# Kernel tuning notes

Hardware: AMD Instinct MI355X
Metric: run time of the kernel (lower is better)

Reference implementation:

```python
import jax, jax.numpy as jnp
import numpy as np

# MambaConfig defaults for d_model=512
N_LAYERS = 2
D_MODEL = 512
ED = 2 * D_MODEL        # d_inner (expand_factor=2)
D_STATE = 16
D_CONV = 4
DT_RANK = D_MODEL // 16  # 32
INPUT_DIM = 64
EPS = 1e-5


def silu(v):
    return v * jax.nn.sigmoid(v)


def rmsnorm(v, w):
    return v * jax.lax.rsqrt(jnp.mean(v * v, axis=-1, keepdims=True) + EPS) * w


def setup_inputs() -> dict:
    key = jax.random.key(0)
    ks = jax.random.split(key, 12)
    B, L = 2, 2048
    s = 0.02
    x = jax.random.normal(ks[0], (B, L, INPUT_DIM), dtype=jnp.float32)
    emb_w = jax.random.normal(ks[1], (D_MODEL, INPUT_DIM), dtype=jnp.float32) * s
    emb_b = jnp.zeros((D_MODEL,), dtype=jnp.float32)
    in_proj_w = jax.random.normal(ks[2], (N_LAYERS, 2 * ED, D_MODEL), dtype=jnp.float32) * s
    conv_w = jax.random.normal(ks[3], (N_LAYERS, ED, D_CONV), dtype=jnp.float32) * 0.2
    conv_b = jax.random.normal(ks[4], (N_LAYERS, ED), dtype=jnp.float32) * 0.02
    x_proj_w = jax.random.normal(ks[5], (N_LAYERS, DT_RANK + 2 * D_STATE, ED), dtype=jnp.float32) * s
    dt_proj_w = jax.random.normal(ks[6], (N_LAYERS, ED, DT_RANK), dtype=jnp.float32) * s
    dt_proj_b = jax.random.normal(ks[7], (N_LAYERS, ED), dtype=jnp.float32) * 0.5 - 4.0  # softplus(~-4) ~ small dt
    A_log = jnp.log(jnp.tile(jnp.arange(1, D_STATE + 1, dtype=jnp.float32), (N_LAYERS, ED, 1)))  # S4D-real init
    D = jnp.ones((N_LAYERS, ED), dtype=jnp.float32)
    out_proj_w = jax.random.normal(ks[8], (N_LAYERS, D_MODEL, ED), dtype=jnp.float32) * s
    norm_w = jnp.ones((N_LAYERS, D_MODEL), dtype=jnp.float32)
    return dict(x=x, emb_w=emb_w, emb_b=emb_b, in_proj_w=in_proj_w, conv_w=conv_w,
                conv_b=conv_b, x_proj_w=x_proj_w, dt_proj_w=dt_proj_w, dt_proj_b=dt_proj_b,
                A_log=A_log, D=D, out_proj_w=out_proj_w, norm_w=norm_w)


def mamba_block(h, in_w, cw, cb, xp_w, dt_w, dt_b, a_log, d_param, out_w):
    B, L, _ = h.shape
    xz = jnp.einsum('bld,ed->ble', h, in_w)            # (B,L,2*ED)
    xi, z = jnp.split(xz, 2, axis=-1)
    # depthwise causal conv along L
    xc = jax.lax.conv_general_dilated(
        xi.transpose(0, 2, 1), cw[:, None, :], (1,), ((D_CONV - 1, 0),),
        dimension_numbers=('NCH', 'OIH', 'NCH'), feature_group_count=ED)
    xi = silu(xc.transpose(0, 2, 1) + cb)              # (B,L,ED)
    dbc = jnp.einsum('ble,ke->blk', xi, xp_w)          # (B,L,dt_rank+2N)
    dt, Bm, Cm = jnp.split(dbc, [DT_RANK, DT_RANK + D_STATE], axis=-1)
    delta = jax.nn.softplus(jnp.einsum('blr,er->ble', dt, dt_w) + dt_b)  # (B,L,ED)
    A = -jnp.exp(a_log)                                # (ED,N)
    dA = jnp.exp(delta[..., None] * A)                 # (B,L,ED,N)
    dBx = (delta * xi)[..., None] * Bm[:, :, None, :]  # (B,L,ED,N)

    def step(hs, inp):
        dA_t, dBx_t, C_t = inp
        hs = dA_t * hs + dBx_t                          # (B,ED,N)
        y_t = jnp.einsum('ben,bn->be', hs, C_t)
        return hs, y_t

    h0 = jnp.zeros((B, ED, D_STATE), dtype=h.dtype)
    _, ys = jax.lax.scan(step, h0, (dA.transpose(1, 0, 2, 3),
                                    dBx.transpose(1, 0, 2, 3),
                                    Cm.transpose(1, 0, 2)))
    y = ys.transpose(1, 0, 2) + d_param * xi
    y = y * silu(z)
    return jnp.einsum('ble,de->bld', y, out_w)


def reference(x, emb_w, emb_b, in_proj_w, conv_w, conv_b, x_proj_w,
              dt_proj_w, dt_proj_b, A_log, D, out_proj_w, norm_w):
    h = jnp.einsum('bli,di->bld', x, emb_w) + emb_b
    for i in range(N_LAYERS):
        h = h + mamba_block(rmsnorm(h, norm_w[i]), in_proj_w[i], conv_w[i], conv_b[i],
                            x_proj_w[i], dt_proj_w[i], dt_proj_b[i],
                            A_log[i], D[i], out_proj_w[i])
    return h
```

## Files before the change

kernel.cpp:

```cpp
#include <hip/hip_runtime.h>
#include <hip/hip_bf16.h>

#define TOKENS   4096
#define BATCH    2
#define LSEQ     2048
#define DM       512
#define EDIM     1024
#define NSTATE   16
#define DCONV    4
#define DTRANK   32
#define TCHUNK   32
#define NCHUNKS  (LSEQ/TCHUNK)
#define KSPLIT   8

typedef unsigned short u16;
typedef __attribute__((ext_vector_type(8))) short bf16x8;
typedef __attribute__((ext_vector_type(4))) float f32x4;

__device__ __forceinline__ u16 f2b(float f){
    union{float f; unsigned u;} v; v.f=f;
    unsigned r = v.u + 0x7FFFu + ((v.u>>16)&1u);
    return (u16)(r>>16);
}
__device__ __forceinline__ float b2f(u16 b){
    union{unsigned u; float f;} v; v.u = ((unsigned)b)<<16; return v.f;
}

template<bool BF>
__device__ __forceinline__ float ld(const void* p, long i) {
    if (BF) return b2f(((const u16*)p)[i]);
    return ((const float*)p)[i];
}
__device__ __forceinline__ float ldf(const void* p, long i, int bf){
    return bf ? b2f(((const u16*)p)[i]) : ((const float*)p)[i];
}

__device__ __forceinline__ float sigmoidf_(float v){ return 1.f/(1.f+__expf(-v)); }
__device__ __forceinline__ float siluf_(float v){ return v*sigmoidf_(v); }
__device__ __forceinline__ float softplusf_(float v){ return v>20.f ? v : __logf(1.f + __expf(v)); }

__global__ void detect_kernel(const void* probe, int* flag){
    unsigned u = *(const unsigned*)probe;
    *flag = (u == 0x3F800000u) ? 0 : 1;
}

__global__ void convall_kernel(const void* s0, u16* d0, long n0,
                               const void* s1, u16* d1, long n1,
                               const void* s2, u16* d2, long n2,
                               const void* s3, u16* d3, long n3,
                               const void* s4, u16* d4, long n4,
                               const int* flag){
    if (*flag) return;
    long i = (long)blockIdx.x*256 + threadIdx.x;
    if (i < n0){ d0[i] = f2b(((const float*)s0)[i]); return; } i -= n0;
    if (i < n1){ d1[i] = f2b(((const float*)s1)[i]); return; } i -= n1;
    if (i < n2){ d2[i] = f2b(((const float*)s2)[i]); return; } i -= n2;
    if (i < n3){ d3[i] = f2b(((const float*)s3)[i]); return; } i -= n3;
    if (i < n4){ d4[i] = f2b(((const float*)s4)[i]); }
}

template<bool BF>
__device__ void rms_body(const float* h, const void* nw, u16* hn, int layer){
    __shared__ float red[256];
    int t = blockIdx.x, tid = threadIdx.x;
    float v0 = h[(long)t*DM + tid];
    float v1 = h[(long)t*DM + 256 + tid];
    red[tid] = v0*v0 + v1*v1;
    __syncthreads();
    for (int off=128; off>0; off>>=1){
        if (tid < off) red[tid] += red[tid+off];
        __syncthreads();
    }
    float scale = rsqrtf(red[0]*(1.0f/DM) + 1e-5f);
    hn[(long)t*DM + tid]       = f2b(v0*scale*ld<BF>(nw, (long)layer*DM + tid));
    hn[(long)t*DM + 256 + tid] = f2b(v1*scale*ld<BF>(nw, (long)layer*DM + 256 + tid));
}
__global__ void rms_kernel(const float* h, const void* nw, u16* hn, int layer, const int* flag){
    if (*flag) rms_body<true>(h,nw,hn,layer); else rms_body<false>(h,nw,hn,layer);
}

template<int MODE>
__global__ __launch_bounds__(256,2)
void gemm128_kernel(const void* Aorig, const u16* __restrict__ Aconv,
                    const void* worig, const u16* __restrict__ wconv,
                    void* Cv, const void* bias, const float* __restrict__ resid,
                    int M, int N, int K, int lda, long boff, const int* flag){
    int bf = *flag;
    const u16* A = bf ? (const u16*)Aorig : Aconv;
    const u16* W = bf ? ((const u16*)worig) + boff : wconv + boff;
    __shared__ u16 As[128*40];
    __shared__ u16 Bs[128*40];
    int t = threadIdx.x;
    int n0 = blockIdx.x*128, m0 = blockIdx.y*128;
    int w = t>>6, lane = t&63;
    int wm = w>>1, wn = w&1;
    int lm = lane&15, lk = lane>>4;
    f32x4 acc[4][4];
    #pragma unroll
    for (int i=0;i<4;i++)
        #pragma unroll
        for (int j=0;j<4;j++) acc[i][j] = (f32x4){0.f,0.f,0.f,0.f};
    int arow = t>>1;
    int aks  = (t&1)*16;
    for (int k0=0; k0<K; k0+=32){
        float4 av0 = *(const float4*)&A[(long)(m0+arow)*lda + k0 + aks];
        float4 av1 = *(const float4*)&A[(long)(m0+arow)*lda + k0 + aks + 8];
        float4 bv0 = *(const float4*)&W[(long)(n0+arow)*K + k0 + aks];
        float4 bv1 = *(const float4*)&W[(long)(n0+arow)*K + k0 + aks + 8];
        __syncthreads();
        *(float4*)&As[arow*40 + aks]     = av0;
        *(float4*)&As[arow*40 + aks + 8] = av1;
        *(float4*)&Bs[arow*40 + aks]     = bv0;
        *(float4*)&Bs[arow*40 + aks + 8] = bv1;
        __syncthreads();
        bf16x8 af[4], bfr[4];
        #pragma unroll
        for (int mi=0;mi<4;mi++) af[mi]  = *(const bf16x8*)&As[(wm*64+mi*16+lm)*40 + lk*8];
        #pragma unroll
        for (int ni=0;ni<4;ni++) bfr[ni] = *(const bf16x8*)&Bs[(wn*64+ni*16+lm)*40 + lk*8];
        #pragma unroll
        for (int mi=0;mi<4;mi++)
            #pragma unroll
            for (int ni=0;ni<4;ni++)
                acc[mi][ni] = __builtin_amdgcn_mfma_f32_16x16x32_bf16(af[mi], bfr[ni], acc[mi][ni], 0,0,0);
    }
    #pragma unroll
    for (int mi=0;mi<4;mi++){
        #pragma unroll
        for (int ni=0;ni<4;ni++){
            int row = m0 + wm*64 + mi*16 + lk*4;
            int col = n0 + wn*64 + ni*16 + lm;
            float bb = (MODE==0) ? ldf(bias, col, bf) : 0.f;
            #pragma unroll
            for (int r=0;r<4;r++){
                long idx = (long)(row+r)*N + col;
                if (MODE==0) ((float*)Cv)[idx] = acc[mi][ni][r] + bb;
                if (MODE==1) ((u16*)Cv)[idx]   = f2b(acc[mi][ni][r]);
                if (MODE==2) ((float*)Cv)[idx] += acc[mi][ni][r];
                if (MODE==3){
                    float v = resid[idx] + acc[mi][ni][r];
                    if (bf) ((u16*)Cv)[idx] = f2b(v);
                    else    ((float*)Cv)[idx] = v;
                }
            }
        }
    }
}

__global__ __launch_bounds__(256,2)
void gemmx_kernel(const u16* __restrict__ A, const void* worig, const u16* __restrict__ wconv,
                  float* __restrict__ part, long boff, const int* flag){
    const u16* W = (*flag) ? ((const u16*)worig) + boff : wconv + boff;
    __shared__ u16 As[128*40];
    __shared__ u16 Bs[64*40];
    int t = threadIdx.x;
    int m0 = blockIdx.x*128;
    int kz = blockIdx.y;
    int w = t>>6, lane = t&63;
    int wm = w>>1, wn = w&1;
    int lm = lane&15, lk = lane>>4;
    f32x4 acc[4][2];
    #pragma unroll
    for (int i=0;i<4;i++){ acc[i][0]=(f32x4){0,0,0,0}; acc[i][1]=(f32x4){0,0,0,0}; }
    int arow = t>>1;
    int aks  = (t&1)*16;
    const int KS = EDIM/KSPLIT;
    for (int it=0; it<KS; it+=32){
        int k0 = kz*KS + it;
        float4 av0 = *(const float4*)&A[(long)(m0+arow)*EDIM + k0 + aks];
        float4 av1 = *(const float4*)&A[(long)(m0+arow)*EDIM + k0 + aks + 8];
        float4 bv0, bv1;
        if (t < 128){
            bv0 = *(const float4*)&W[(long)arow*EDIM + k0 + aks];
            bv1 = *(const float4*)&W[(long)arow*EDIM + k0 + aks + 8];
        }
        __syncthreads();
        *(float4*)&As[arow*40 + aks]     = av0;
        *(float4*)&As[arow*40 + aks + 8] = av1;
        if (t < 128){
            *(float4*)&Bs[arow*40 + aks]     = bv0;
            *(float4*)&Bs[arow*40 + aks + 8] = bv1;
        }
        __syncthreads();
        bf16x8 af[4], bfr[2];
        #pragma unroll
        for (int mi=0;mi<4;mi++) af[mi]  = *(const bf16x8*)&As[(wm*64+mi*16+lm)*40 + lk*8];
        #pragma unroll
        for (int ni=0;ni<2;ni++) bfr[ni] = *(const bf16x8*)&Bs[(wn*32+ni*16+lm)*40 + lk*8];
        #pragma unroll
        for (int mi=0;mi<4;mi++)
            #pragma unroll
            for (int ni=0;ni<2;ni++)
                acc[mi][ni] = __builtin_amdgcn_mfma_f32_16x16x32_bf16(af[mi], bfr[ni], acc[mi][ni], 0,0,0);
    }
    #pragma unroll
    for (int mi=0;mi<4;mi++){
        #pragma unroll
        for (int ni=0;ni<2;ni++){
            int row = m0 + wm*64 + mi*16 + lk*4;
            int col = wn*32 + ni*16 + lm;
            #pragma unroll
            for (int r=0;r<4;r++)
                part[((long)kz*TOKENS + row + r)*64 + col] = acc[mi][ni][r];
        }
    }
}

__global__ void reduce_dbc_kernel(const float* __restrict__ part, float* __restrict__ dbc){
    long i = (long)blockIdx.x*256 + threadIdx.x;
    float s = 0.f;
    #pragma unroll
    for (int z=0; z<KSPLIT; z++) s += part[(long)z*TOKENS*64 + i];
    dbc[i] = s;
}

template<bool BF>
__device__ void conv_body(const u16* xz, const void* cw, const void* cb, u16* xic, int layer){
    long idx = (long)blockIdx.x*256 + threadIdx.x;
    int t = (int)(idx >> 10), e = (int)(idx & (EDIM-1));
    int l = t & (LSEQ-1);
    long wo = ((long)layer*EDIM + e)*DCONV;
    float w0=ld<BF>(cw,wo+0), w1=ld<BF>(cw,wo+1), w2=ld<BF>(cw,wo+2), w3=ld<BF>(cw,wo+3);
    float s = ld<BF>(cb, (long)layer*EDIM + e);
    if (l-3 >= 0) s = fmaf(b2f(xz[(long)(t-3)*2048 + e]), w0, s);
    if (l-2 >= 0) s = fmaf(b2f(xz[(long)(t-2)*2048 + e]), w1, s);
    if (l-1 >= 0) s = fmaf(b2f(xz[(long)(t-1)*2048 + e]), w2, s);
    s = fmaf(b2f(xz[(long)t*2048 + e]), w3, s);
    xic[idx] = f2b(siluf_(s));
}
__global__ void conv_kernel(const u16* xz, const void* cw, const void* cb, u16* xic, int layer, const int* flag){
    if (*flag) conv_body<true>(xz,cw,cb,xic,layer); else conv_body<false>(xz,cw,cb,xic,layer);
}

template<bool BF>
__device__ void phase1_body(const float* __restrict__ dbc, const u16* __restrict__ xic,
                            const void* A_log, const void* dtw, const void* dtb,
                            float* __restrict__ chunkP, float* __restrict__ chunkL, int layer){
    int lane = threadIdx.x;
    int ch = blockIdx.x*64 + lane;
    int b = ch >> 10, e = ch & (EDIM-1);
    int c = blockIdx.y;
    float w[DTRANK];
    long wo = ((long)layer*EDIM + e)*DTRANK;
    #pragma unroll
    for (int r=0;r<DTRANK;r++) w[r] = ld<BF>(dtw, wo+r);
    float bias = ld<BF>(dtb, (long)layer*EDIM + e);
    float a[NSTATE];
    long ao = ((long)layer*EDIM + e)*NSTATE;
    #pragma unroll
    for (int n=0;n<NSTATE;n++) a[n] = -__expf(ld<BF>(A_log, ao+n));
    float P[NSTATE], L[NSTATE];
    #pragma unroll
    for (int n=0;n<NSTATE;n++){ P[n]=1.f; L[n]=0.f; }
    long tok0 = (long)b*LSEQ + (long)c*TCHUNK;
    for (int i=0;i<TCHUNK;i++){
        long tok = tok0 + i;
        const float4* row4 = (const float4*)(dbc + tok*64);
        float rr[DTRANK];
        #pragma unroll
        for (int q=0;q<8;q++){ float4 v=row4[q]; rr[q*4]=v.x; rr[q*4+1]=v.y; rr[q*4+2]=v.z; rr[q*4+3]=v.w; }
        float Bv[NSTATE];
        #pragma unroll
        for (int q=0;q<4;q++){ float4 v=row4[8+q]; Bv[q*4]=v.x; Bv[q*4+1]=v.y; Bv[q*4+2]=v.z; Bv[q*4+3]=v.w; }
        float s = bias;
        #pragma unroll
        for (int r=0;r<DTRANK;r++) s = fmaf(rr[r], w[r], s);
        float delta = softplusf_(s);
        float xv = b2f(xic[tok*EDIM + e]);
        float dx = delta * xv;
        #pragma unroll
        for (int n=0;n<NSTATE;n++){
            float dA = __expf(delta * a[n]);
            P[n] *= dA;
            L[n] = fmaf(dA, L[n], dx * Bv[n]);
        }
    }
    long g = ((long)b*NCHUNKS + c)*EDIM*NSTATE + (long)e*NSTATE;
    #pragma unroll
    for (int n=0;n<NSTATE;n+=4){
        *(float4*)&chunkP[g+n] = make_float4(P[n],P[n+1],P[n+2],P[n+3]);
        *(float4*)&chunkL[g+n] = make_float4(L[n],L[n+1],L[n+2],L[n+3]);
    }
}
__global__ void phase1_kernel(const float* dbc, const u16* xic, const void* A_log,
                              const void* dtw, const void* dtb,
                              float* chunkP, float* chunkL, int layer, const int* flag){
    if (*flag) phase1_body<true>(dbc,xic,A_log,dtw,dtb,chunkP,chunkL,layer);
    else       phase1_body<false>(dbc,xic,A_log,dtw,dtb,chunkP,chunkL,layer);
}

__global__ void phase2_kernel(float* chunkP, const float* __restrict__ chunkL){
    int tid = blockIdx.x*256 + threadIdx.x;
    int q  = (tid & 3)*4;
    int ch = tid >> 2;
    int b = ch >> 10, e = ch & (EDIM-1);
    float4 h = make_float4(0,0,0,0);
    for (int c=0;c<NCHUNKS;c++){
        long g = ((long)(b*NCHUNKS + c)*EDIM + e)*NSTATE + q;
        float4 P = *(const float4*)&chunkP[g];
        float4 L = *(const float4*)&chunkL[g];
        *(float4*)&chunkP[g] = h;
        h.x = fmaf(P.x, h.x, L.x);
        h.y = fmaf(P.y, h.y, L.y);
        h.z = fmaf(P.z, h.z, L.z);
        h.w = fmaf(P.w, h.w, L.w);
    }
}

template<bool BF>
__device__ void phase3_body(const float* __restrict__ dbc, const u16* __restrict__ xic,
                            const u16* __restrict__ xzb, u16* __restrict__ ybf,
                            const float* __restrict__ chunkP,
                            const void* A_log, const void* dtw, const void* dtb,
                            const void* Dp, int layer){
    int lane = threadIdx.x;
    int ch = blockIdx.x*64 + lane;
    int b = ch >> 10, e = ch & (EDIM-1);
    int c = blockIdx.y;
    float w[DTRANK];
    long wo = ((long)layer*EDIM + e)*DTRANK;
    #pragma unroll
    for (int r=0;r<DTRANK;r++) w[r] = ld<BF>(dtw, wo+r);
    float bias = ld<BF>(dtb, (long)layer*EDIM + e);
    float a[NSTATE];
    long ao = ((long)layer*EDIM + e)*NSTATE;
    #pragma unroll
    for (int n=0;n<NSTATE;n++) a[n] = -__expf(ld<BF>(A_log, ao+n));
    float D_e = ld<BF>(Dp, (long)layer*EDIM + e);
    float h[NSTATE];
    long g = ((long)b*NCHUNKS + c)*EDIM*NSTATE + (long)e*NSTATE;
    #pragma unroll
    for (int q=0;q<NSTATE;q+=4){
        float4 v = *(const float4*)&chunkP[g+q];
        h[q]=v.x; h[q+1]=v.y; h[q+2]=v.z; h[q+3]=v.w;
    }
    long tok0 = (long)b*LSEQ + (long)c*TCHUNK;
    for (int i=0;i<TCHUNK;i++){
        long tok = tok0 + i;
        const float4* row4 = (const float4*)(dbc + tok*64);
        float rr[DTRANK];
        #pragma unroll
        for (int q=0;q<8;q++){ float4 v=row4[q]; rr[q*4]=v.x; rr[q*4+1]=v.y; rr[q*4+2]=v.z; rr[q*4+3]=v.w; }
        float Bv[NSTATE], Cv[NSTATE];
        #pragma unroll
        for (int q=0;q<4;q++){ float4 v=row4[8+q];  Bv[q*4]=v.x; Bv[q*4+1]=v.y; Bv[q*4+2]=v.z; Bv[q*4+3]=v.w; }
        #pragma unroll
        for (int q=0;q<4;q++){ float4 v=row4[12+q]; Cv[q*4]=v.x; Cv[q*4+1]=v.y; Cv[q*4+2]=v.z; Cv[q*4+3]=v.w; }
        float s = bias;
        #pragma unroll
        for (int r=0;r<DTRANK;r++) s = fmaf(rr[r], w[r], s);
        float delta = softplusf_(s);
        float xv = b2f(xic[tok*EDIM + e]);
        float zv = b2f(xzb[tok*2048 + EDIM + e]);
        float dx = delta * xv;
        float acc = D_e * xv;
        #pragma unroll
        for (int n=0;n<NSTATE;n++){
            float dA = __expf(delta * a[n]);
            h[n] = fmaf(dA, h[n], dx * Bv[n]);
            acc = fmaf(h[n], Cv[n], acc);
        }
        ybf[tok*EDIM + e] = f2b(acc * siluf_(zv));
    }
}
__global__ void phase3_kernel(const float* dbc, const u16* xic, const u16* xzb, u16* ybf,
                              const float* chunkP, const void* A_log, const void* dtw,
                              const void* dtb, const void* Dp, int layer, const int* flag){
    if (*flag) phase3_body<true>(dbc,xic,xzb,ybf,chunkP,A_log,dtw,dtb,Dp,layer);
    else       phase3_body<false>(dbc,xic,xzb,ybf,chunkP,A_log,dtw,dtb,Dp,layer);
}

extern "C" void kernel_launch(void* const* d_in, const int* in_sizes, int n_in,
                              void* d_out, int out_size, void* d_ws, size_t ws_size,
                              hipStream_t stream){
    const void* x       = d_in[0];
    const void* emb_w   = d_in[1];
    const void* emb_b   = d_in[2];
    const void* in_w    = d_in[3];
    const void* conv_w  = d_in[4];
    const void* conv_b  = d_in[5];
    const void* xp_w    = d_in[6];
    const void* dt_w    = d_in[7];
    const void* dt_b    = d_in[8];
    const void* A_log   = d_in[9];
    const void* Dp      = d_in[10];
    const void* out_w   = d_in[11];
    const void* norm_w  = d_in[12];

    const long N_X   = (long)TOKENS*64;
    const long N_EW  = (long)DM*64;
    const long N_IN  = (long)2*2*EDIM*DM;
    const long N_XP  = (long)2*64*EDIM;
    const long N_OUT = (long)2*DM*EDIM;

    char* ws = (char*)d_ws;
    int*   flag    = (int*)ws;
    float* h       = (float*)(ws + 256);
    u16*   hn      = (u16*)  (h      + (long)TOKENS*DM);
    u16*   xzb     = hn      + (long)TOKENS*DM;
    u16*   xic     = xzb     + (long)TOKENS*2*EDIM;
    u16*   ybf     = xic     + (long)TOKENS*EDIM;
    float* dbc     = (float*)(ybf + (long)TOKENS*EDIM);
    float* dpart   = dbc     + (long)TOKENS*64;
    float* chunkP  = dpart   + (long)KSPLIT*TOKENS*64;
    float* chunkL  = chunkP  + (long)BATCH*NCHUNKS*EDIM*NSTATE;
    u16*   w_in    = (u16*)  (chunkL + (long)BATCH*NCHUNKS*EDIM*NSTATE);
    u16*   w_xp    = w_in    + N_IN;
    u16*   w_out   = w_xp    + N_XP;
    u16*   x_cv    = w_out   + N_OUT;
    u16*   ew_cv   = x_cv    + N_X;

    detect_kernel<<<1, 1, 0, stream>>>(norm_w, flag);
    {
        long ntot = N_X + N_EW + N_IN + N_XP + N_OUT;
        convall_kernel<<<(int)((ntot+255)/256), 256, 0, stream>>>(
            x, x_cv, N_X,  emb_w, ew_cv, N_EW,  in_w, w_in, N_IN,
            xp_w, w_xp, N_XP,  out_w, w_out, N_OUT,  flag);
    }

    gemm128_kernel<0><<<dim3(DM/128, TOKENS/128), 256, 0, stream>>>(
        x, x_cv, emb_w, ew_cv, h, emb_b, nullptr, TOKENS, DM, 64, 64, 0, flag);

    for (int layer = 0; layer < 2; layer++){
        rms_kernel<<<TOKENS, 256, 0, stream>>>(h, norm_w, hn, layer, flag);

        gemm128_kernel<1><<<dim3(2*EDIM/128, TOKENS/128), 256, 0, stream>>>(
            hn, hn, in_w, w_in, xzb, nullptr, nullptr,
            TOKENS, 2*EDIM, DM, DM, (long)layer*2*EDIM*DM, flag);

        conv_kernel<<<(TOKENS*EDIM)/256, 256, 0, stream>>>(xzb, conv_w, conv_b, xic, layer, flag);

        gemmx_kernel<<<dim3(TOKENS/128, KSPLIT), 256, 0, stream>>>(
            xic, xp_w, w_xp, dpart, (long)layer*64*EDIM, flag);
        reduce_dbc_kernel<<<(TOKENS*64)/256, 256, 0, stream>>>(dpart, dbc);

        phase1_kernel<<<dim3((BATCH*EDIM)/64, NCHUNKS), 64, 0, stream>>>(
            dbc, xic, A_log, dt_w, dt_b, chunkP, chunkL, layer, flag);
        phase2_kernel<<<(BATCH*EDIM*4)/256, 256, 0, stream>>>(chunkP, chunkL);
        phase3_kernel<<<dim3((BATCH*EDIM)/64, NCHUNKS), 64, 0, stream>>>(
            dbc, xic, xzb, ybf, chunkP, A_log, dt_w, dt_b, Dp, layer, flag);

        if (layer == 0){
            gemm128_kernel<2><<<dim3(DM/128, TOKENS/128), 256, 0, stream>>>(
                ybf, ybf, out_w, w_out, h, nullptr, nullptr,
                TOKENS, DM, EDIM, EDIM, 0L, flag);
        } else {
            gemm128_kernel<3><<<dim3(DM/128, TOKENS/128), 256, 0, stream>>>(
                ybf, ybf, out_w, w_out, d_out, nullptr, h,
                TOKENS, DM, EDIM, EDIM, (long)DM*EDIM, flag);
        }
    }
}
```

Before: 448.4 us.

## Vectorize elementwise kernels and use async global-to-LDS loads in GEMM

Several unrelated changes: the fp32-to-bf16 conversion kernel becomes grid-stride with a fixed grid, RMSNorm uses one wavefront per token with shuffle reduction and 8-wide loads and stores, the conv and dbc-reduce kernels process 8 and 4 elements per thread with vector accesses, and the 128x128 GEMM fills shared memory with global_load_lds direct copies instead of register staging. The aim is fewer memory instructions, less reduction sync, and less register traffic in the GEMM. The GEMM drops the padded LDS stride (40 to 32), so the fragment reads may hit bank conflicts, and the direct-to-LDS layout depends on how lanes map their 16-byte writes.

After: 423.7 us. 1.06x faster.

```diff
diff --git a/kernel.cpp b/kernel.cpp
--- a/kernel.cpp
+++ b/kernel.cpp
@@ -15,7 +15,12 @@
 
 typedef unsigned short u16;
 typedef __attribute__((ext_vector_type(8))) short bf16x8;
+typedef __attribute__((ext_vector_type(8))) unsigned short u16x8;
 typedef __attribute__((ext_vector_type(4))) float f32x4;
+
+#define ASYNC_CP16(gptr, lptr) \
+    __builtin_amdgcn_global_load_lds((const __attribute__((address_space(1))) void*)(gptr), \
+                                     (__attribute__((address_space(3))) void*)(lptr), 16, 0, 0)
 
 __device__ __forceinline__ u16 f2b(float f){
     union{float f; unsigned u;} v; v.f=f;
@@ -51,29 +56,33 @@
                                const void* s4, u16* d4, long n4,
                                const int* flag){
     if (*flag) return;
-    long i = (long)blockIdx.x*256 + threadIdx.x;
-    if (i < n0){ d0[i] = f2b(((const float*)s0)[i]); return; } i -= n0;
-    if (i < n1){ d1[i] = f2b(((const float*)s1)[i]); return; } i -= n1;
-    if (i < n2){ d2[i] = f2b(((const float*)s2)[i]); return; } i -= n2;
-    if (i < n3){ d3[i] = f2b(((const float*)s3)[i]); return; } i -= n3;
-    if (i < n4){ d4[i] = f2b(((const float*)s4)[i]); }
+    long ntot = n0+n1+n2+n3+n4;
+    for (long i = (long)blockIdx.x*256 + threadIdx.x; i < ntot; i += (long)gridDim.x*256){
+        long j = i;
+        if (j < n0){ d0[j] = f2b(((const float*)s0)[j]); continue; } j -= n0;
+        if (j < n1){ d1[j] = f2b(((const float*)s1)[j]); continue; } j -= n1;
+        if (j < n2){ d2[j] = f2b(((const float*)s2)[j]); continue; } j -= n2;
+        if (j < n3){ d3[j] = f2b(((const float*)s3)[j]); continue; } j -= n3;
+        d4[j] = f2b(((const float*)s4)[j]);
+    }
 }
 
 template<bool BF>
 __device__ void rms_body(const float* h, const void* nw, u16* hn, int layer){
-    __shared__ float red[256];
-    int t = blockIdx.x, tid = threadIdx.x;
-    float v0 = h[(long)t*DM + tid];
-    float v1 = h[(long)t*DM + 256 + tid];
-    red[tid] = v0*v0 + v1*v1;
-    __syncthreads();
-    for (int off=128; off>0; off>>=1){
-        if (tid < off) red[tid] += red[tid+off];
-        __syncthreads();
-    }
-    float scale = rsqrtf(red[0]*(1.0f/DM) + 1e-5f);
-    hn[(long)t*DM + tid]       = f2b(v0*scale*ld<BF>(nw, (long)layer*DM + tid));
-    hn[(long)t*DM + 256 + tid] = f2b(v1*scale*ld<BF>(nw, (long)layer*DM + 256 + tid));
+    int wv = threadIdx.x>>6, lane = threadIdx.x&63;
+    int t = blockIdx.x*4 + wv;
+    long base = (long)t*DM + lane*8;
+    float4 a = *(const float4*)&h[base];
+    float4 b = *(const float4*)&h[base+4];
+    float s = a.x*a.x+a.y*a.y+a.z*a.z+a.w*a.w + b.x*b.x+b.y*b.y+b.z*b.z+b.w*b.w;
+    #pragma unroll
+    for (int off=1; off<64; off<<=1) s += __shfl_xor(s, off);
+    float scale = rsqrtf(s*(1.0f/DM) + 1e-5f);
+    float v[8] = {a.x,a.y,a.z,a.w,b.x,b.y,b.z,b.w};
+    u16x8 o;
+    #pragma unroll
+    for (int j=0;j<8;j++) o[j] = f2b(v[j]*scale*ld<BF>(nw, (long)layer*DM + lane*8 + j));
+    *(u16x8*)&hn[base] = o;
 }
 __global__ void rms_kernel(const float* h, const void* nw, u16* hn, int layer, const int* flag){
     if (*flag) rms_body<true>(h,nw,hn,layer); else rms_body<false>(h,nw,hn,layer);
@@ -88,36 +97,36 @@
     int bf = *flag;
     const u16* A = bf ? (const u16*)Aorig : Aconv;
     const u16* W = bf ? ((const u16*)worig) + boff : wconv + boff;
-    __shared__ u16 As[128*40];
-    __shared__ u16 Bs[128*40];
+    __shared__ u16 As[128*32];
+    __shared__ u16 Bs[128*32];
     int t = threadIdx.x;
     int n0 = blockIdx.x*128, m0 = blockIdx.y*128;
     int w = t>>6, lane = t&63;
     int wm = w>>1, wn = w&1;
     int lm = lane&15, lk = lane>>4;
+    int srow = w*16 + (lane>>2);
+    int seg8 = (lane&3)*8;
+    u16* lbaseA1 = As + w*512;
+    u16* lbaseA2 = As + 2048 + w*512;
+    u16* lbaseB1 = Bs + w*512;
+    u16* lbaseB2 = Bs + 2048 + w*512;
     f32x4 acc[4][4];
     #pragma unroll
     for (int i=0;i<4;i++)
         #pragma unroll
         for (int j=0;j<4;j++) acc[i][j] = (f32x4){0.f,0.f,0.f,0.f};
-    int arow = t>>1;
-    int aks  = (t&1)*16;
     for (int k0=0; k0<K; k0+=32){
-        float4 av0 = *(const float4*)&A[(long)(m0+arow)*lda + k0 + aks];
-        float4 av1 = *(const float4*)&A[(long)(m0+arow)*lda + k0 + aks + 8];
-        float4 bv0 = *(const float4*)&W[(long)(n0+arow)*K + k0 + aks];
-        float4 bv1 = *(const float4*)&W[(long)(n0+arow)*K + k0 + aks + 8];
         __syncthreads();
-        *(float4*)&As[arow*40 + aks]     = av0;
-        *(float4*)&As[arow*40 + aks + 8] = av1;
-        *(float4*)&Bs[arow*40 + aks]     = bv0;
-        *(float4*)&Bs[arow*40 + aks + 8] = bv1;
+        ASYNC_CP16(&A[(long)(m0+srow)*lda + k0 + seg8],      lbaseA1);
+        ASYNC_CP16(&A[(long)(m0+64+srow)*lda + k0 + seg8],   lbaseA2);
+        ASYNC_CP16(&W[(long)(n0+srow)*K + k0 + seg8],        lbaseB1);
+        ASYNC_CP16(&W[(long)(n0+64+srow)*K + k0 + seg8],     lbaseB2);
         __syncthreads();
         bf16x8 af[4], bfr[4];
         #pragma unroll
-        for (int mi=0;mi<4;mi++) af[mi]  = *(const bf16x8*)&As[(wm*64+mi*16+lm)*40 + lk*8];
-        #pragma unroll
-        for (int ni=0;ni<4;ni++) bfr[ni] = *(const bf16x8*)&Bs[(wn*64+ni*16+lm)*40 + lk*8];
+        for (int mi=0;mi<4;mi++) af[mi]  = *(const bf16x8*)&As[(wm*64+mi*16+lm)*32 + lk*8];
+        #pragma unroll
+        for (int ni=0;ni<4;ni++) bfr[ni] = *(const bf16x8*)&Bs[(wn*64+ni*16+lm)*32 + lk*8];
         #pragma unroll
         for (int mi=0;mi<4;mi++)
             #pragma unroll
@@ -207,26 +216,39 @@
 }
 
 __global__ void reduce_dbc_kernel(const float* __restrict__ part, float* __restrict__ dbc){
-    long i = (long)blockIdx.x*256 + threadIdx.x;
-    float s = 0.f;
-    #pragma unroll
-    for (int z=0; z<KSPLIT; z++) s += part[(long)z*TOKENS*64 + i];
-    dbc[i] = s;
+    long i = ((long)blockIdx.x*256 + threadIdx.x)*4;
+    float4 s = *(const float4*)&part[i];
+    #pragma unroll
+    for (int z=1; z<KSPLIT; z++){
+        float4 p = *(const float4*)&part[(long)z*TOKENS*64 + i];
+        s.x += p.x; s.y += p.y; s.z += p.z; s.w += p.w;
+    }
+    *(float4*)&dbc[i] = s;
 }
 
 template<bool BF>
 __device__ void conv_body(const u16* xz, const void* cw, const void* cb, u16* xic, int layer){
     long idx = (long)blockIdx.x*256 + threadIdx.x;
-    int t = (int)(idx >> 10), e = (int)(idx & (EDIM-1));
+    int t = (int)(idx >> 7), e0 = (int)((idx & 127)*8);
     int l = t & (LSEQ-1);
-    long wo = ((long)layer*EDIM + e)*DCONV;
-    float w0=ld<BF>(cw,wo+0), w1=ld<BF>(cw,wo+1), w2=ld<BF>(cw,wo+2), w3=ld<BF>(cw,wo+3);
-    float s = ld<BF>(cb, (long)layer*EDIM + e);
-    if (l-3 >= 0) s = fmaf(b2f(xz[(long)(t-3)*2048 + e]), w0, s);
-    if (l-2 >= 0) s = fmaf(b2f(xz[(long)(t-2)*2048 + e]), w1, s);
-    if (l-1 >= 0) s = fmaf(b2f(xz[(long)(t-1)*2048 + e]), w2, s);
-    s = fmaf(b2f(xz[(long)t*2048 + e]), w3, s);
-    xic[idx] = f2b(siluf_(s));
+    u16x8 r0 = {0,0,0,0,0,0,0,0}, r1 = r0, r2 = r0;
+    if (l >= 3) r0 = *(const u16x8*)&xz[(long)(t-3)*2048 + e0];
+    if (l >= 2) r1 = *(const u16x8*)&xz[(long)(t-2)*2048 + e0];
+    if (l >= 1) r2 = *(const u16x8*)&xz[(long)(t-1)*2048 + e0];
+    u16x8 r3 = *(const u16x8*)&xz[(long)t*2048 + e0];
+    u16x8 o;
+    #pragma unroll
+    for (int j=0;j<8;j++){
+        int e = e0 + j;
+        long wo = ((long)layer*EDIM + e)*DCONV;
+        float s = ld<BF>(cb, (long)layer*EDIM + e);
+        s = fmaf(b2f(r0[j]), ld<BF>(cw,wo+0), s);
+        s = fmaf(b2f(r1[j]), ld<BF>(cw,wo+1), s);
+        s = fmaf(b2f(r2[j]), ld<BF>(cw,wo+2), s);
+        s = fmaf(b2f(r3[j]), ld<BF>(cw,wo+3), s);
+        o[j] = f2b(siluf_(s));
+    }
+    *(u16x8*)&xic[(long)t*EDIM + e0] = o;
 }
 __global__ void conv_kernel(const u16* xz, const void* cw, const void* cb, u16* xic, int layer, const int* flag){
     if (*flag) conv_body<true>(xz,cw,cb,xic,layer); else conv_body<false>(xz,cw,cb,xic,layer);
@@ -411,28 +433,25 @@
     u16*   ew_cv   = x_cv    + N_X;
 
     detect_kernel<<<1, 1, 0, stream>>>(norm_w, flag);
-    {
-        long ntot = N_X + N_EW + N_IN + N_XP + N_OUT;
-        convall_kernel<<<(int)((ntot+255)/256), 256, 0, stream>>>(
-            x, x_cv, N_X,  emb_w, ew_cv, N_EW,  in_w, w_in, N_IN,
-            xp_w, w_xp, N_XP,  out_w, w_out, N_OUT,  flag);
-    }
+    convall_kernel<<<4096, 256, 0, stream>>>(
+        x, x_cv, N_X,  emb_w, ew_cv, N_EW,  in_w, w_in, N_IN,
+        xp_w, w_xp, N_XP,  out_w, w_out, N_OUT,  flag);
 
     gemm128_kernel<0><<<dim3(DM/128, TOKENS/128), 256, 0, stream>>>(
         x, x_cv, emb_w, ew_cv, h, emb_b, nullptr, TOKENS, DM, 64, 64, 0, flag);
 
     for (int layer = 0; layer < 2; layer++){
-        rms_kernel<<<TOKENS, 256, 0, stream>>>(h, norm_w, hn, layer, flag);
+        rms_kernel<<<TOKENS/4, 256, 0, stream>>>(h, norm_w, hn, layer, flag);
 
         gemm128_kernel<1><<<dim3(2*EDIM/128, TOKENS/128), 256, 0, stream>>>(
             hn, hn, in_w, w_in, xzb, nullptr, nullptr,
             TOKENS, 2*EDIM, DM, DM, (long)layer*2*EDIM*DM, flag);
 
-        conv_kernel<<<(TOKENS*EDIM)/256, 256, 0, stream>>>(xzb, conv_w, conv_b, xic, layer, flag);
+        conv_kernel<<<(TOKENS*EDIM)/(256*8), 256, 0, stream>>>(xzb, conv_w, conv_b, xic, layer, flag);
 
         gemmx_kernel<<<dim3(TOKENS/128, KSPLIT), 256, 0, stream>>>(
             xic, xp_w, w_xp, dpart, (long)layer*64*EDIM, flag);
-        reduce_dbc_kernel<<<(TOKENS*64)/256, 256, 0, stream>>>(dpart, dbc);
+        reduce_dbc_kernel<<<(TOKENS*64)/(256*4), 256, 0, stream>>>(dpart, dbc);
 
         phase1_kernel<<<dim3((BATCH*EDIM)/64, NCHUNKS), 64, 0, stream>>>(
             dbc, xic, A_log, dt_w, dt_b, chunkP, chunkL, layer, flag);
```
